# Performance work log

Hardware: AMD Instinct MI355X
Metric: run time of the kernel (lower is better)

Reference implementation:

```python
import jax, jax.numpy as jnp
import numpy as np

B, T, D = 2, 2048, 1024   # batch, seq, d_model
E, K, H = 8, 2, 704       # routed experts, topk, expert hidden
SH = 704 * 2              # shared-expert hidden = moe_hidden * num_shared_experts
EPS = 1e-20               # topk_norm_epsilon
STD = 0.02                # init_weight_std


def setup_inputs() -> dict:
    key = jax.random.key(0)
    ks = jax.random.split(key, 8)
    return {
        "x":   jax.random.normal(ks[0], (B, T, D), jnp.float32),
        "Wg":  jax.random.normal(ks[1], (E, D), jnp.float32) * STD,   # router experts_weights
        "W1":  jax.random.normal(ks[2], (E, D, H), jnp.float32) * STD,  # gate proj per expert
        "W3":  jax.random.normal(ks[3], (E, D, H), jnp.float32) * STD,  # up proj per expert
        "W2":  jax.random.normal(ks[4], (E, H, D), jnp.float32) * STD,  # down proj per expert
        "Ws1": jax.random.normal(ks[5], (D, SH), jnp.float32) * STD,    # shared expert
        "Ws3": jax.random.normal(ks[6], (D, SH), jnp.float32) * STD,
        "Ws2": jax.random.normal(ks[7], (SH, D), jnp.float32) * STD,
    }


def reference(x, Wg, W1, W3, W2, Ws1, Ws3, Ws2):
    b, t, d = x.shape
    n = b * t
    xf = x.reshape(n, d)
    # softmax gating + topk + scatter back into dense [N,E] gate matrix
    gates = jax.nn.softmax(xf @ Wg.T, axis=-1)                      # [N,E]
    top_v, top_i = jax.lax.top_k(gates, K)                          # [N,K]
    masked = jnp.zeros_like(gates).at[jnp.arange(n)[:, None], top_i].set(top_v)
    masked = masked / (masked.sum(-1, keepdims=True) + EPS)         # normalized_moe_gates
    # per-expert SwiGLU FFN over all tokens, then gate-weighted combine
    h = jnp.einsum('nd,edh->enh', xf, W1)                           # [E,N,H]
    g = jnp.einsum('nd,edh->enh', xf, W3)
    y = jnp.einsum('enh,ehd->end', jax.nn.silu(h) * g, W2)          # [E,N,D]
    routed = jnp.einsum('ne,end->nd', masked, y)                    # combine
    shared = (jax.nn.silu(xf @ Ws1) * (xf @ Ws3)) @ Ws2             # shared experts
    return (routed + shared).reshape(b, t, d)
```

## Files before the change

### kernel.cpp

```cpp
#include <hip/hip_runtime.h>
#include <math.h>

typedef __bf16 bf16;
typedef __attribute__((ext_vector_type(8))) __bf16 bf16x8;
typedef __attribute__((ext_vector_type(4))) __bf16 bf16x4;
typedef __attribute__((ext_vector_type(4))) float f32x4;

#define NTOK 4096
#define DM   1024
#define NE   8
#define NEX  10
#define HE   704

#define MAP1_CAP 224
#define MAP2_CAP 128

#define OFF_CNT   0u
#define OFF_TOK   256u
#define OFF_WGT   131328u
#define OFF_XB    262400u
#define OFF_W1T   8651008u
#define OFF_W3T   20185344u
#define OFF_W2T   31719680u
#define OFF_WS1T  43254016u
#define OFF_WS3T  46137600u
#define OFF_WS2T  49021184u
#define OFF_ACT   51904768u
#define OFF_EIDS  74973440u
#define OFF_MAP1  OFF_EIDS
#define OFF_MAP2  (OFF_EIDS + 8192u)
#define OFF_GW    74989824u
#define OFF_SLOT  75022592u
#define OFF_YR    OFF_W1T

__device__ __forceinline__ void async_cp16(const bf16* g, bf16* l)
{
    __builtin_amdgcn_global_load_lds(
        (const __attribute__((address_space(1))) unsigned int*)g,
        (__attribute__((address_space(3))) unsigned int*)l, 16, 0, 0);
}

__global__ void cvt_x_kernel(const float* __restrict__ x, bf16* __restrict__ xb, int n4)
{
    int i = blockIdx.x * blockDim.x + threadIdx.x;
    if (i >= n4) return;
    float4 v = ((const float4*)x)[i];
    bf16x4 o;
    o[0] = (bf16)v.x; o[1] = (bf16)v.y; o[2] = (bf16)v.z; o[3] = (bf16)v.w;
    ((bf16x4*)xb)[i] = o;
}

__global__ __launch_bounds__(256) void transpose_all(
    const float* __restrict__ W1, const float* __restrict__ W3, const float* __restrict__ W2,
    const float* __restrict__ Ws1, const float* __restrict__ Ws3, const float* __restrict__ Ws2,
    bf16* __restrict__ w1t, bf16* __restrict__ w3t, bf16* __restrict__ w2t,
    bf16* __restrict__ ws1t, bf16* __restrict__ ws3t, bf16* __restrict__ ws2t)
{
    int id = blockIdx.x;
    const float* src; bf16* dst; int C, rt, ct, nkt;
    if (id < 5632)       { int t = id;         int e = t / 704, m = t % 704; C = 704;
                           src = W1 + (size_t)e * 1024 * 704;  dst = w1t + (size_t)e * 720896;
                           ct = m % 22; rt = m / 22; nkt = 32; }
    else if (id < 11264) { int t = id - 5632;  int e = t / 704, m = t % 704; C = 704;
                           src = W3 + (size_t)e * 1024 * 704;  dst = w3t + (size_t)e * 720896;
                           ct = m % 22; rt = m / 22; nkt = 32; }
    else if (id < 16896) { int t = id - 11264; int e = t / 704, m = t % 704; C = 1024;
                           src = W2 + (size_t)e * 704 * 1024;  dst = w2t + (size_t)e * 720896;
                           ct = m % 32; rt = m / 32; nkt = 22; }
    else if (id < 18304) { int t = id - 16896; C = 1408; src = Ws1;
                           ct = t % 44; rt = t / 44; nkt = 32;
                           int ep = (ct >= 22) ? 1 : 0; ct -= 22 * ep;
                           src += (size_t)704 * ep;
                           dst = ws1t + (size_t)ep * 720896; }
    else if (id < 19712) { int t = id - 18304; C = 1408; src = Ws3;
                           ct = t % 44; rt = t / 44; nkt = 32;
                           int ep = (ct >= 22) ? 1 : 0; ct -= 22 * ep;
                           src += (size_t)704 * ep;
                           dst = ws3t + (size_t)ep * 720896; }
    else                 { int t = id - 19712; C = 1024; src = Ws2;
                           ct = t % 32; rt = t / 32; nkt = 22;
                           int ep = (rt >= 22) ? 1 : 0; rt -= 22 * ep;
                           src += (size_t)704 * 1024 * ep;
                           dst = ws2t + (size_t)ep * 720896; }

    __shared__ float tl[32][33];
    int c0 = ct * 32, r0 = rt * 32;
    int row  = threadIdx.x >> 3;
    int col4 = (threadIdx.x & 7) * 4;
    float4 v = *(const float4*)&src[(size_t)(r0 + row) * C + c0 + col4];
    tl[row][col4 + 0] = v.x; tl[row][col4 + 1] = v.y;
    tl[row][col4 + 2] = v.z; tl[row][col4 + 3] = v.w;
    __syncthreads();
    int n  = c0 + row;
    int ng = n >> 4, nr = n & 15;
    int kt = rt;
    int cc = col4 >> 3, j = col4 & 7;
    bf16x4 o;
    o[0] = (bf16)tl[col4 + 0][row];
    o[1] = (bf16)tl[col4 + 1][row];
    o[2] = (bf16)tl[col4 + 2][row];
    o[3] = (bf16)tl[col4 + 3][row];
    *(bf16x4*)&dst[(size_t)(((ng * nkt + kt) << 9) + (((cc << 4) | nr) << 3) + j)] = o;
}

__global__ __launch_bounds__(256) void router_logits(
    const float* __restrict__ x, const float* __restrict__ Wg,
    int* __restrict__ eids, float2* __restrict__ gw)
{
    int n    = blockIdx.x * 4 + (threadIdx.x >> 6);
    int lane = threadIdx.x & 63;
    const float* xrow = x + (size_t)n * DM;
    float xr[16];
    #pragma unroll
    for (int j = 0; j < 16; j++) xr[j] = xrow[lane + 64 * j];
    float logit[NE];
    #pragma unroll
    for (int e = 0; e < NE; e++) {
        const float* wr = Wg + e * DM;
        float s = 0.f;
        #pragma unroll
        for (int j = 0; j < 16; j++) s += xr[j] * wr[lane + 64 * j];
        #pragma unroll
        for (int off = 32; off; off >>= 1) s += __shfl_xor(s, off, 64);
        logit[e] = s;
    }
    if (lane == 0) {
        int i0 = 0;
        #pragma unroll
        for (int e = 1; e < NE; e++) if (logit[e] > logit[i0]) i0 = e;
        int i1 = (i0 == 0) ? 1 : 0;
        #pragma unroll
        for (int e = 0; e < NE; e++) if (e != i0 && logit[e] > logit[i1]) i1 = e;
        float m = logit[0];
        #pragma unroll
        for (int e = 1; e < NE; e++) m = fmaxf(m, logit[e]);
        float denom = 0.f;
        #pragma unroll
        for (int e = 0; e < NE; e++) denom += expf(logit[e] - m);
        float g0 = expf(logit[i0] - m) / denom;
        float g1 = expf(logit[i1] - m) / denom;
        float inv = 1.f / (g0 + g1 + 1e-20f);
        eids[n] = i0 | (i1 << 16);
        gw[n] = make_float2(g0 * inv, g1 * inv);
    }
}

__global__ __launch_bounds__(128) void build_lists(
    const int* __restrict__ eids, const float2* __restrict__ gw,
    int* __restrict__ cnt, int* __restrict__ tok, float* __restrict__ wgt,
    int2* __restrict__ slots)
{
    __shared__ int lcnt[NE];
    __shared__ int gbase[NE];
    int t = threadIdx.x;
    int n = blockIdx.x * 128 + t;
    if (t < NE) lcnt[t] = 0;
    __syncthreads();
    int packed = eids[n];
    float2 w = gw[n];
    int e0 = packed & 0xffff, e1 = packed >> 16;
    int s0 = atomicAdd(&lcnt[e0], 1);
    int s1 = atomicAdd(&lcnt[e1], 1);
    __syncthreads();
    if (t < NE) gbase[t] = atomicAdd(&cnt[t], lcnt[t]);
    __syncthreads();
    int p0 = gbase[e0] + s0, p1 = gbase[e1] + s1;
    tok[e0 * NTOK + p0] = n; wgt[e0 * NTOK + p0] = w.x;
    tok[e1 * NTOK + p1] = n; wgt[e1 * NTOK + p1] = w.y;
    slots[n] = make_int2((e0 << 16) | p0, (e1 << 16) | p1);
}

__global__ void prefix_kernel(const int* __restrict__ cnt, int* __restrict__ pfx,
                              int* __restrict__ map1, int* __restrict__ map2)
{
    int t = threadIdx.x;
    for (int i = t; i < 8 * MAP1_CAP; i += 64) map1[i] = -1;
    for (int i = t; i < 8 * MAP2_CAP; i += 64) map2[i] = -1;
    __syncthreads();
    if (t != 0) return;
    int s = 0;
    for (int e = 0; e < NEX; e++) { pfx[e] = s; s += (e < NE) ? cnt[e] : NTOK; }
    pfx[NEX] = s;

    int ntl[NEX];
    int tot1 = 0;
    for (int e = 0; e < NEX; e++) {
        int c = (e < NE) ? cnt[e] : NTOK;
        ntl[e] = (c + 127) >> 7;
        tot1 += ntl[e];
    }
    {
        int len[8] = {0,0,0,0,0,0,0,0};
        int avg = (tot1 * 11 + 7) >> 3;
        int k = 0;
        for (int e = 0; e < NEX; e++) {
            k = 0;
            for (int q = 1; q < 8; q++) if (len[q] < len[k]) k = q;
            for (int tt = 0; tt < ntl[e]; tt++) {
                if (len[k] >= avg) {
                    k = 0;
                    for (int q = 1; q < 8; q++) if (len[q] < len[k]) k = q;
                }
                for (int h = 0; h < 11; h++)
                    map1[(len[k] + h) * 8 + k] = (e << 20) | (tt << 8) | h;
                len[k] += 11;
            }
        }
    }
    {
        int len[8] = {0,0,0,0,0,0,0,0};
        int tot2 = 0;
        for (int e = 0; e <= NE; e++) tot2 += (e < NE) ? ntl[e] : (NTOK >> 7);
        int avg = tot2;
        int k = 0;
        for (int e = 0; e <= NE; e++) {
            int nt2 = (e < NE) ? ntl[e] : (NTOK >> 7);
            k = 0;
            for (int q = 1; q < 8; q++) if (len[q] < len[k]) k = q;
            for (int tt = 0; tt < nt2; tt++) {
                if (len[k] >= avg) {
                    k = 0;
                    for (int q = 1; q < 8; q++) if (len[q] < len[k]) k = q;
                }
                for (int d = 0; d < 8; d++)
                    map2[(len[k] + d) * 8 + k] = (e << 20) | (tt << 8) | d;
                len[k] += 8;
            }
        }
    }
}

__global__ __launch_bounds__(256) void gemm1_swiglu(
    const bf16* __restrict__ xb,
    const bf16* __restrict__ w1t, const bf16* __restrict__ w3t,
    const bf16* __restrict__ ws1t, const bf16* __restrict__ ws3t,
    bf16* __restrict__ act,
    const int* __restrict__ cnt, const int* __restrict__ pfx,
    const int* __restrict__ tok, const int* __restrict__ map)
{
    int b = blockIdx.x;
    int ent = map[(b >> 3) * 8 + (b & 7)];
    if (ent < 0) return;
    int e  = ent >> 20;
    int m0 = ((ent >> 8) & 0xfff) << 7;
    int h0 = (ent & 255) * 64;
    int count = (e < NE) ? cnt[e] : NTOK;
    int base = pfx[e];
    const bf16 *B1, *B3;
    if (e < NE) { B1 = w1t + (size_t)e * 720896;         B3 = w3t + (size_t)e * 720896; }
    else        { B1 = ws1t + (size_t)(e - NE) * 720896; B3 = ws3t + (size_t)(e - NE) * 720896; }
    const int* tlist = (e < NE) ? tok + e * NTOK : nullptr;

    __shared__ bf16 As[2][8 * 512];
    __shared__ bf16 B1s[2][4 * 512];
    __shared__ bf16 B3s[2][4 * 512];

    int tid = threadIdx.x, w = tid >> 6, lane = tid & 63;

    int r3 = lane >> 2;
    int cx = (lane & 3) ^ ((r3 >> 1) & 3);
    int sA0 = m0 + 32 * w + r3, sA1 = sA0 + 16;
    int rA0 = tlist ? (sA0 < count ? tlist[sA0] : 0) : (sA0 < count ? sA0 : 0);
    int rA1 = tlist ? (sA1 < count ? tlist[sA1] : 0) : (sA1 < count ? sA1 : 0);
    const bf16* ga0 = xb + (size_t)rA0 * DM + cx * 8;
    const bf16* ga1 = xb + (size_t)rA1 * DM + cx * 8;
    const bf16* gb1 = B1 + ((size_t)((h0 >> 4) + w) * 32) * 512 + lane * 8;
    const bf16* gb3 = B3 + ((size_t)((h0 >> 4) + w) * 32) * 512 + lane * 8;
    bf16* aA0 = &As[0][0]  + (2 * w) * 512;
    bf16* aA1 = aA0 + 512;
    bf16* aB1 = &B1s[0][0] + w * 512;
    bf16* aB3 = &B3s[0][0] + w * 512;

    int rl = lane & 15, ch = lane >> 4;
    int uA = 4 * rl + (ch ^ ((rl >> 1) & 3));
    int gA = (w & 1) * 4;
    int gB = (w >> 1) * 2;
    int wm = (w & 1) * 64, wn = (w >> 1) * 32;

    f32x4 acch[4][2], accg[4][2];
    #pragma unroll
    for (int i = 0; i < 4; i++)
        #pragma unroll
        for (int j = 0; j < 2; j++) {
            acch[i][j] = (f32x4){0.f, 0.f, 0.f, 0.f};
            accg[i][j] = (f32x4){0.f, 0.f, 0.f, 0.f};
        }

#define STAGE1(buf) do { \
        async_cp16(ga0, aA0 + (buf) * 4096); \
        async_cp16(ga1, aA1 + (buf) * 4096); \
        async_cp16(gb1, aB1 + (buf) * 2048); \
        async_cp16(gb3, aB3 + (buf) * 2048); \
        ga0 += 32; ga1 += 32; gb1 += 512; gb3 += 512; \
    } while (0)

    STAGE1(0);
    __syncthreads();
    for (int k0 = 0; k0 < 32; k0++) {
        int cur = k0 & 1;
        if (k0 < 31) STAGE1(cur ^ 1);
        const bf16* Ab  = &As[0][0]  + cur * 4096;
        const bf16* B1b = &B1s[0][0] + cur * 2048;
        const bf16* B3b = &B3s[0][0] + cur * 2048;
        bf16x8 af[4], b1f[2], b3f[2];
        #pragma unroll
        for (int i = 0; i < 4; i++) af[i] = *(const bf16x8*)(Ab + (gA + i) * 512 + uA * 8);
        #pragma unroll
        for (int j = 0; j < 2; j++) {
            b1f[j] = *(const bf16x8*)(B1b + (gB + j) * 512 + lane * 8);
            b3f[j] = *(const bf16x8*)(B3b + (gB + j) * 512 + lane * 8);
        }
        #pragma unroll
        for (int i = 0; i < 4; i++)
            #pragma unroll
            for (int j = 0; j < 2; j++) {
                acch[i][j] = __builtin_amdgcn_mfma_f32_16x16x32_bf16(af[i], b1f[j], acch[i][j], 0, 0, 0);
                accg[i][j] = __builtin_amdgcn_mfma_f32_16x16x32_bf16(af[i], b3f[j], accg[i][j], 0, 0, 0);
            }
        __syncthreads();
    }
#undef STAGE1

    #pragma unroll
    for (int i = 0; i < 4; i++)
        #pragma unroll
        for (int j = 0; j < 2; j++)
            #pragma unroll
            for (int r = 0; r < 4; r++) {
                int row = wm + i * 16 + ch * 4 + r;
                int s2 = m0 + row;
                if (s2 < count) {
                    float hv = acch[i][j][r], gv = accg[i][j][r];
                    float a = hv / (1.f + expf(-hv)) * gv;
                    act[(size_t)(base + s2) * HE + h0 + wn + j * 16 + rl] = (bf16)a;
                }
            }
}

__global__ __launch_bounds__(256) void gemm2_all(
    const bf16* __restrict__ act,
    const bf16* __restrict__ w2t, const bf16* __restrict__ ws2t,
    bf16* __restrict__ yr, float* __restrict__ out,
    const int* __restrict__ cnt, const int* __restrict__ pfx,
    const float* __restrict__ wgt, const int* __restrict__ map)
{
    int b = blockIdx.x;
    int ent = map[(b >> 3) * 8 + (b & 7)];
    if (ent < 0) return;
    int e  = ent >> 20;
    int m0 = ((ent >> 8) & 0xfff) << 7;
    int d0 = (ent & 255) * 128;

    __shared__ bf16 As[2][8 * 512];
    __shared__ bf16 Bs[2][8 * 512];

    int tid = threadIdx.x, w = tid >> 6, lane = tid & 63;

    int r3 = lane >> 2;
    int cx = (lane & 3) ^ ((r3 >> 1) & 3);
    int sA0 = m0 + 32 * w + r3, sA1 = sA0 + 16;
    int rl = lane & 15, ch = lane >> 4;
    int uA = 4 * rl + (ch ^ ((rl >> 1) & 3));
    int gA = (w & 1) * 4, gB = (w >> 1) * 4;
    int wm = (w & 1) * 64, wn = (w >> 1) * 64;

    bf16* aA0 = &As[0][0] + (2 * w) * 512;
    bf16* aA1 = aA0 + 512;
    bf16* aB0 = &Bs[0][0] + (2 * w) * 512;
    bf16* aB1 = aB0 + 512;

    int count, base; const bf16* Bp;
    if (e < NE) { count = cnt[e]; base = pfx[e]; Bp = w2t + (size_t)e * 720896; }
    else        { count = NTOK;   base = NTOK * 2; Bp = ws2t; }

    int a0 = (sA0 < count) ? (base + sA0) : base;
    int a1 = (sA1 < count) ? (base + sA1) : base;
    const bf16* ga0 = act + (size_t)a0 * HE + cx * 8;
    const bf16* ga1 = act + (size_t)a1 * HE + cx * 8;
    const bf16* gb0 = Bp + ((size_t)((d0 >> 4) + 2 * w) * 22) * 512 + lane * 8;
    const bf16* gb1 = Bp + ((size_t)((d0 >> 4) + 2 * w + 1) * 22) * 512 + lane * 8;

    f32x4 acc[4][4];
    #pragma unroll
    for (int i = 0; i < 4; i++)
        #pragma unroll
        for (int j = 0; j < 4; j++) acc[i][j] = (f32x4){0.f, 0.f, 0.f, 0.f};

#define STAGE2(buf) do { \
        async_cp16(ga0, aA0 + (buf) * 4096); \
        async_cp16(ga1, aA1 + (buf) * 4096); \
        async_cp16(gb0, aB0 + (buf) * 4096); \
        async_cp16(gb1, aB1 + (buf) * 4096); \
        ga0 += 32; ga1 += 32; gb0 += 512; gb1 += 512; \
    } while (0)

    int total = (e < NE) ? 22 : 44;
    STAGE2(0);
    int ns = 1;
    __syncthreads();
    for (int kt = 0; kt < total; kt++) {
        int cur = kt & 1;
        if (ns < total) {
            if (ns == 22) {
                ga0 = act + (size_t)(12288 + sA0) * HE + cx * 8;
                ga1 = act + (size_t)(12288 + sA1) * HE + cx * 8;
                const bf16* B2 = ws2t + 720896;
                gb0 = B2 + ((size_t)((d0 >> 4) + 2 * w) * 22) * 512 + lane * 8;
                gb1 = B2 + ((size_t)((d0 >> 4) + 2 * w + 1) * 22) * 512 + lane * 8;
            }
            STAGE2(cur ^ 1);
            ns++;
        }
        const bf16* Ab = &As[0][0] + cur * 4096;
        const bf16* Bb = &Bs[0][0] + cur * 4096;
        bf16x8 af[4], bf_[4];
        #pragma unroll
        for (int i = 0; i < 4; i++) af[i]  = *(const bf16x8*)(Ab + (gA + i) * 512 + uA * 8);
        #pragma unroll
        for (int j = 0; j < 4; j++) bf_[j] = *(const bf16x8*)(Bb + (gB + j) * 512 + lane * 8);
        #pragma unroll
        for (int i = 0; i < 4; i++)
            #pragma unroll
            for (int j = 0; j < 4; j++)
                acc[i][j] = __builtin_amdgcn_mfma_f32_16x16x32_bf16(af[i], bf_[j], acc[i][j], 0, 0, 0);
        __syncthreads();
    }
#undef STAGE2

    if (e < NE) {
        const float* wl = wgt + e * NTOK;
        #pragma unroll
        for (int i = 0; i < 4; i++) {
            #pragma unroll
            for (int r = 0; r < 4; r++) {
                int row = wm + i * 16 + ch * 4 + r;
                int s2 = m0 + row;
                if (s2 < count) {
                    float wt = wl[s2];
                    bf16* yrow = yr + (size_t)(base + s2) * DM + d0 + wn;
                    #pragma unroll
                    for (int j = 0; j < 4; j++)
                        yrow[j * 16 + rl] = (bf16)(wt * acc[i][j][r]);
                }
            }
        }
    } else {
        #pragma unroll
        for (int i = 0; i < 4; i++) {
            #pragma unroll
            for (int r = 0; r < 4; r++) {
                int row = wm + i * 16 + ch * 4 + r;
                float* orow = out + (size_t)(m0 + row) * DM + d0 + wn;
                #pragma unroll
                for (int j = 0; j < 4; j++)
                    orow[j * 16 + rl] = acc[i][j][r];
            }
        }
    }
}

__global__ __launch_bounds__(256) void fuse_add(
    const bf16* __restrict__ yr, const int2* __restrict__ slots,
    const int* __restrict__ pfx, float* __restrict__ out)
{
    int n = blockIdx.x;
    int2 s = slots[n];
    int slot0 = pfx[s.x >> 16] + (s.x & 0xffff);
    int slot1 = pfx[s.y >> 16] + (s.y & 0xffff);
    const bf16* y0 = yr + (size_t)slot0 * DM;
    const bf16* y1 = yr + (size_t)slot1 * DM;
    float* orow = out + (size_t)n * DM;
    int d = threadIdx.x * 4;
    bf16x4 a = *(const bf16x4*)(y0 + d);
    bf16x4 b = *(const bf16x4*)(y1 + d);
    float4 o = *(float4*)(orow + d);
    o.x += (float)a[0] + (float)b[0];
    o.y += (float)a[1] + (float)b[1];
    o.z += (float)a[2] + (float)b[2];
    o.w += (float)a[3] + (float)b[3];
    *(float4*)(orow + d) = o;
}

extern "C" void kernel_launch(void* const* d_in, const int* in_sizes, int n_in,
                              void* d_out, int out_size, void* d_ws, size_t ws_size,
                              hipStream_t stream)
{
    const float* x   = (const float*)d_in[0];
    const float* Wg  = (const float*)d_in[1];
    const float* W1  = (const float*)d_in[2];
    const float* W3  = (const float*)d_in[3];
    const float* W2  = (const float*)d_in[4];
    const float* Ws1 = (const float*)d_in[5];
    const float* Ws3 = (const float*)d_in[6];
    const float* Ws2 = (const float*)d_in[7];
    float* out = (float*)d_out;
    char*  ws  = (char*)d_ws;

    int*    cnt   = (int*)(ws + OFF_CNT);
    int*    pfx   = (int*)(ws + OFF_CNT + 32);
    int*    tok   = (int*)(ws + OFF_TOK);
    float*  wgt   = (float*)(ws + OFF_WGT);
    bf16*   xb    = (bf16*)(ws + OFF_XB);
    bf16*   w1t   = (bf16*)(ws + OFF_W1T);
    bf16*   w3t   = (bf16*)(ws + OFF_W3T);
    bf16*   w2t   = (bf16*)(ws + OFF_W2T);
    bf16*   ws1t  = (bf16*)(ws + OFF_WS1T);
    bf16*   ws3t  = (bf16*)(ws + OFF_WS3T);
    bf16*   ws2t  = (bf16*)(ws + OFF_WS2T);
    bf16*   act   = (bf16*)(ws + OFF_ACT);
    int*    eids  = (int*)(ws + OFF_EIDS);
    int*    map1  = (int*)(ws + OFF_MAP1);
    int*    map2  = (int*)(ws + OFF_MAP2);
    float2* gw    = (float2*)(ws + OFF_GW);
    int2*   slots = (int2*)(ws + OFF_SLOT);
    bf16*   yr    = (bf16*)(ws + OFF_YR);

    hipMemsetAsync(ws, 0, 256, stream);

    cvt_x_kernel<<<4096, 256, 0, stream>>>(x, xb, NTOK * DM / 4);
    transpose_all<<<21120, 256, 0, stream>>>(W1, W3, W2, Ws1, Ws3, Ws2,
                                             w1t, w3t, w2t, ws1t, ws3t, ws2t);
    router_logits<<<1024, 256, 0, stream>>>(x, Wg, eids, gw);
    build_lists<<<32, 128, 0, stream>>>(eids, gw, cnt, tok, wgt, slots);
    prefix_kernel<<<1, 64, 0, stream>>>(cnt, pfx, map1, map2);

    gemm1_swiglu<<<8 * MAP1_CAP, 256, 0, stream>>>(
        xb, w1t, w3t, ws1t, ws3t, act, cnt, pfx, tok, map1);

    gemm2_all<<<8 * MAP2_CAP, 256, 0, stream>>>(
        act, w2t, ws2t, yr, out, cnt, pfx, wgt, map2);

    fuse_add<<<NTOK, 256, 0, stream>>>(yr, slots, pfx, out);
}
```

Baseline: 357.2 us.

## Triple-buffer LDS staging in both MoE GEMMs with explicit vmcnt waits

Both GEMM kernels move from double to triple buffering of shared-memory tiles, so loads are issued two K-steps ahead. The full __syncthreads is replaced by a partial vmcnt wait and a raw s_barrier, which lets one stage of async copies stay in flight across the barrier. This is meant to hide global-memory latency behind MFMA work, at the cost of 50% more LDS per block and possibly lower occupancy. Correctness now depends on the hand-counted vmcnt values matching the async copies each stage issues.

```diff
diff --git a/kernel.cpp b/kernel.cpp
--- a/kernel.cpp
+++ b/kernel.cpp
@@ -251,9 +251,9 @@
     else        { B1 = ws1t + (size_t)(e - NE) * 720896; B3 = ws3t + (size_t)(e - NE) * 720896; }
     const int* tlist = (e < NE) ? tok + e * NTOK : nullptr;
 
-    __shared__ bf16 As[2][8 * 512];
-    __shared__ bf16 B1s[2][4 * 512];
-    __shared__ bf16 B3s[2][4 * 512];
+    __shared__ bf16 As[3][8 * 512];
+    __shared__ bf16 B1s[3][4 * 512];
+    __shared__ bf16 B3s[3][4 * 512];
 
     int tid = threadIdx.x, w = tid >> 6, lane = tid & 63;
 
@@ -286,22 +286,24 @@
             accg[i][j] = (f32x4){0.f, 0.f, 0.f, 0.f};
         }
 
-#define STAGE1(buf) do { \
-        async_cp16(ga0, aA0 + (buf) * 4096); \
-        async_cp16(ga1, aA1 + (buf) * 4096); \
-        async_cp16(gb1, aB1 + (buf) * 2048); \
-        async_cp16(gb3, aB3 + (buf) * 2048); \
+#define STAGE1(bs) do { \
+        async_cp16(ga0, aA0 + (bs) * 4096); \
+        async_cp16(ga1, aA1 + (bs) * 4096); \
+        async_cp16(gb1, aB1 + (bs) * 2048); \
+        async_cp16(gb3, aB3 + (bs) * 2048); \
         ga0 += 32; ga1 += 32; gb1 += 512; gb3 += 512; \
     } while (0)
 
     STAGE1(0);
-    __syncthreads();
+    STAGE1(1);
+    asm volatile("s_waitcnt vmcnt(4)" ::: "memory");
+    __builtin_amdgcn_s_barrier();
+
+    int rb = 0, sb = 2;
     for (int k0 = 0; k0 < 32; k0++) {
-        int cur = k0 & 1;
-        if (k0 < 31) STAGE1(cur ^ 1);
-        const bf16* Ab  = &As[0][0]  + cur * 4096;
-        const bf16* B1b = &B1s[0][0] + cur * 2048;
-        const bf16* B3b = &B3s[0][0] + cur * 2048;
+        const bf16* Ab  = &As[0][0]  + rb * 4096;
+        const bf16* B1b = &B1s[0][0] + rb * 2048;
+        const bf16* B3b = &B3s[0][0] + rb * 2048;
         bf16x8 af[4], b1f[2], b3f[2];
         #pragma unroll
         for (int i = 0; i < 4; i++) af[i] = *(const bf16x8*)(Ab + (gA + i) * 512 + uA * 8);
@@ -310,6 +312,7 @@
             b1f[j] = *(const bf16x8*)(B1b + (gB + j) * 512 + lane * 8);
             b3f[j] = *(const bf16x8*)(B3b + (gB + j) * 512 + lane * 8);
         }
+        if (k0 < 30) STAGE1(sb);
         #pragma unroll
         for (int i = 0; i < 4; i++)
             #pragma unroll
@@ -317,7 +320,12 @@
                 acch[i][j] = __builtin_amdgcn_mfma_f32_16x16x32_bf16(af[i], b1f[j], acch[i][j], 0, 0, 0);
                 accg[i][j] = __builtin_amdgcn_mfma_f32_16x16x32_bf16(af[i], b3f[j], accg[i][j], 0, 0, 0);
             }
-        __syncthreads();
+        if (k0 < 30)       asm volatile("s_waitcnt vmcnt(4)" ::: "memory");
+        else if (k0 == 30) asm volatile("s_waitcnt vmcnt(0)" ::: "memory");
+        __builtin_amdgcn_sched_barrier(0);
+        __builtin_amdgcn_s_barrier();
+        rb = (rb == 2) ? 0 : rb + 1;
+        sb = (sb == 2) ? 0 : sb + 1;
     }
 #undef STAGE1
 
@@ -351,8 +359,8 @@
     int m0 = ((ent >> 8) & 0xfff) << 7;
     int d0 = (ent & 255) * 128;
 
-    __shared__ bf16 As[2][8 * 512];
-    __shared__ bf16 Bs[2][8 * 512];
+    __shared__ bf16 As[3][8 * 512];
+    __shared__ bf16 Bs[3][8 * 512];
 
     int tid = threadIdx.x, w = tid >> 6, lane = tid & 63;
 
@@ -386,44 +394,51 @@
         #pragma unroll
         for (int j = 0; j < 4; j++) acc[i][j] = (f32x4){0.f, 0.f, 0.f, 0.f};
 
-#define STAGE2(buf) do { \
-        async_cp16(ga0, aA0 + (buf) * 4096); \
-        async_cp16(ga1, aA1 + (buf) * 4096); \
-        async_cp16(gb0, aB0 + (buf) * 4096); \
-        async_cp16(gb1, aB1 + (buf) * 4096); \
+#define STAGE2(bs) do { \
+        async_cp16(ga0, aA0 + (bs) * 4096); \
+        async_cp16(ga1, aA1 + (bs) * 4096); \
+        async_cp16(gb0, aB0 + (bs) * 4096); \
+        async_cp16(gb1, aB1 + (bs) * 4096); \
         ga0 += 32; ga1 += 32; gb0 += 512; gb1 += 512; \
     } while (0)
 
     int total = (e < NE) ? 22 : 44;
     STAGE2(0);
-    int ns = 1;
-    __syncthreads();
+    STAGE2(1);
+    asm volatile("s_waitcnt vmcnt(4)" ::: "memory");
+    __builtin_amdgcn_s_barrier();
+
+    int rb = 0, sb = 2;
     for (int kt = 0; kt < total; kt++) {
-        int cur = kt & 1;
-        if (ns < total) {
-            if (ns == 22) {
+        const bf16* Ab = &As[0][0] + rb * 4096;
+        const bf16* Bb = &Bs[0][0] + rb * 4096;
+        bf16x8 af[4], bf_[4];
+        #pragma unroll
+        for (int i = 0; i < 4; i++) af[i]  = *(const bf16x8*)(Ab + (gA + i) * 512 + uA * 8);
+        #pragma unroll
+        for (int j = 0; j < 4; j++) bf_[j] = *(const bf16x8*)(Bb + (gB + j) * 512 + lane * 8);
+        int nx = kt + 2;
+        if (nx < total) {
+            if (nx == 22) {
                 ga0 = act + (size_t)(12288 + sA0) * HE + cx * 8;
                 ga1 = act + (size_t)(12288 + sA1) * HE + cx * 8;
                 const bf16* B2 = ws2t + 720896;
                 gb0 = B2 + ((size_t)((d0 >> 4) + 2 * w) * 22) * 512 + lane * 8;
                 gb1 = B2 + ((size_t)((d0 >> 4) + 2 * w + 1) * 22) * 512 + lane * 8;
             }
-            STAGE2(cur ^ 1);
-            ns++;
-        }
-        const bf16* Ab = &As[0][0] + cur * 4096;
-        const bf16* Bb = &Bs[0][0] + cur * 4096;
-        bf16x8 af[4], bf_[4];
-        #pragma unroll
-        for (int i = 0; i < 4; i++) af[i]  = *(const bf16x8*)(Ab + (gA + i) * 512 + uA * 8);
-        #pragma unroll
-        for (int j = 0; j < 4; j++) bf_[j] = *(const bf16x8*)(Bb + (gB + j) * 512 + lane * 8);
+            STAGE2(sb);
+        }
         #pragma unroll
         for (int i = 0; i < 4; i++)
             #pragma unroll
             for (int j = 0; j < 4; j++)
                 acc[i][j] = __builtin_amdgcn_mfma_f32_16x16x32_bf16(af[i], bf_[j], acc[i][j], 0, 0, 0);
-        __syncthreads();
+        if (nx < total)       asm volatile("s_waitcnt vmcnt(4)" ::: "memory");
+        else if (nx == total) asm volatile("s_waitcnt vmcnt(0)" ::: "memory");
+        __builtin_amdgcn_sched_barrier(0);
+        __builtin_amdgcn_s_barrier();
+        rb = (rb == 2) ? 0 : rb + 1;
+        sb = (sb == 2) ? 0 : sb + 1;
     }
 #undef STAGE2
 
```

Result: faster. 337.3 us (-5.5%).
